# Kernel optimization log

Hardware: AMD Instinct MI355X
Metric: run time of the kernel (lower is better)

The kernel has to match this reference:

```python
import jax, jax.numpy as jnp
import numpy as np

N_ITER = 5  # from init_kwargs


def setup_inputs() -> dict:
    key = jax.random.key(0)
    k1, k2 = jax.random.split(key)
    K, F, B = 4, 513, 4000
    Xr = jax.random.normal(k1, (K, F, B), dtype=jnp.float32)
    Xi = jax.random.normal(k2, (K, F, B), dtype=jnp.float32)
    return {"Xr": Xr, "Xi": Xi}


def _auxiva(X):
    # X: complex64 (K, F, B)
    K, F, B = X.shape
    # XXh[i,j,f,b] = X[i,f,b] * conj(X[j,f,b])
    XXh = jnp.einsum('ifb,jfb->ijfb', X, X.conj())
    Wh = jnp.tile(jnp.eye(K, dtype=X.dtype)[None], (F, 1, 1))  # (F, K, K)
    for _ in range(N_ITER):
        Y = jnp.einsum('fsc,cfb->sfb', Wh, X)          # demix: (K, F, B)
        r = jnp.linalg.norm(Y, axis=1)                  # (K, B), real
        phi = 1.0 / (2.0 * r)                           # laplace contrast
        # V[k,i,j,f] = mean_b phi[k,b] * XXh[i,j,f,b]  (avoid (K,K,K,F,B) blowup)
        V = jnp.einsum('kb,ijfb->kijf', phi.astype(X.dtype), XXh) / B
        for k in range(K):                              # sequential IP updates
            M = jnp.einsum('fik,kjf->fij', Wh, V[k])    # (F, K, K)
            w = jnp.linalg.inv(M)[:, :, k].conj()       # (F, K)
            denom = jnp.sqrt(jnp.einsum('fc,ckf,fk->f', w, V[k], w.conj()))
            Wh = Wh.at[:, k, :].set(w / denom[:, None])
    Y = jnp.einsum('fsc,cfb->sfb', Wh, X)
    scale = jnp.linalg.inv(Wh)[:, :, 0]                 # projection back: (F, K)
    return jnp.einsum('sfb,fs->sfb', Y, scale)


def reference(Xr, Xi):
    X = (Xr + 1j * Xi).astype(jnp.complex64)
    return _auxiva(X)
```

## Files before the change

kernel.cpp:

```cpp
#include <hip/hip_runtime.h>
#include <hip/hip_bf16.h>
#include <math.h>

#define K 4
#define F 513
#define B 4000
#define NIT 5
#define FB (F*B)
#define KB (K*B)
#define FCH 8
#define NFC 65

__device__ float2 g_Wh[F*16];
__device__ float2 g_V[64*F];
__device__ float2 g_scale[F*4];
__device__ float  g_r2p[NFC*KB];
__device__ float  g_r2[KB];

struct cd { double re, im; };
__device__ inline cd mkcd(double r, double i){ cd z; z.re=r; z.im=i; return z; }
__device__ inline cd cmul(cd a, cd b){ return mkcd(a.re*b.re - a.im*b.im, a.re*b.im + a.im*b.re); }
__device__ inline cd cadd(cd a, cd b){ return mkcd(a.re+b.re, a.im+b.im); }
__device__ inline cd csub(cd a, cd b){ return mkcd(a.re-b.re, a.im-b.im); }
__device__ inline cd conj_(cd a){ return mkcd(a.re, -a.im); }
__device__ inline cd cdiv(cd a, cd b){
  double d = b.re*b.re + b.im*b.im;
  return mkcd((a.re*b.re + a.im*b.im)/d, (a.im*b.re - a.re*b.im)/d);
}

__device__ inline void invcol4(const cd M[4][4], int kk, cd x[4]){
  int r0 = (kk==0)?1:0;
  int r1 = (kk<=1)?2:1;
  int r2 = (kk<=2)?3:2;
  cd cof[4];
  #pragma unroll
  for (int i=0;i<4;++i){
    int c0 = (i==0)?1:0;
    int c1 = (i<=1)?2:1;
    int c2 = (i<=2)?3:2;
    cd m = cadd(csub(cmul(M[r0][c0], csub(cmul(M[r1][c1],M[r2][c2]), cmul(M[r1][c2],M[r2][c1]))),
                     cmul(M[r0][c1], csub(cmul(M[r1][c0],M[r2][c2]), cmul(M[r1][c2],M[r2][c0])))),
                cmul(M[r0][c2], csub(cmul(M[r1][c0],M[r2][c1]), cmul(M[r1][c1],M[r2][c0]))));
    if ((kk+i)&1) m = mkcd(-m.re,-m.im);
    cof[i] = m;
  }
  cd det = mkcd(0.0,0.0);
  #pragma unroll
  for (int i=0;i<4;++i) det = cadd(det, cmul(M[kk][i], cof[i]));
  cd idet = cdiv(mkcd(1.0,0.0), det);
  #pragma unroll
  for (int i=0;i<4;++i) x[i] = cmul(cof[i], idet);
}


__global__ void init_kernel(){
  int t = blockIdx.x*blockDim.x + threadIdx.x;
  if (t < F*16){
    int sc = t & 15; int s = sc >> 2, c = sc & 3;
    g_Wh[t] = make_float2(s==c ? 1.0f : 0.0f, 0.0f);
  }
}

__global__ __launch_bounds__(256) void demix_part_kernel(
    const float* __restrict__ Xr, const float* __restrict__ Xi){
  int b = blockIdx.x*blockDim.x + threadIdx.x;
  if (b >= B) return;
  int y = blockIdx.y;
  int f0 = y*FCH, f1 = min(f0+FCH, F);
  float acc[K];
  #pragma unroll
  for (int s=0;s<K;++s) acc[s]=0.0f;
  for (int f=f0; f<f1; ++f){
    float xr[K], xi[K];
    #pragma unroll
    for (int c=0;c<K;++c){ int idx=c*FB + f*B + b; xr[c]=Xr[idx]; xi[c]=Xi[idx]; }
    const float2* w = g_Wh + f*16;
    #pragma unroll
    for (int s=0;s<K;++s){
      float yr=0.0f, yi=0.0f;
      #pragma unroll
      for (int c=0;c<K;++c){
        float2 ww = w[s*4+c];
        yr += ww.x*xr[c] - ww.y*xi[c];
        yi += ww.x*xi[c] + ww.y*xr[c];
      }
      acc[s] += yr*yr + yi*yi;
    }
  }
  #pragma unroll
  for (int s=0;s<K;++s) g_r2p[y*KB + s*B + b] = acc[s];
}

__global__ __launch_bounds__(256) void reduce_r2_kernel(){
  int t = blockIdx.x*blockDim.x + threadIdx.x;
  if (t >= KB) return;
  float s = 0.0f;
  #pragma unroll 5
  for (int y=0; y<NFC; ++y) s += g_r2p[y*KB + t];
  g_r2[t] = s;
}

__global__ __launch_bounds__(256) void v_kernel(
    const float* __restrict__ Xr, const float* __restrict__ Xi){
  int f = blockIdx.x;
  int tid = threadIdx.x;
  float acc[64];
  #pragma unroll
  for (int q=0;q<64;++q) acc[q]=0.0f;

  for (int b=tid; b<B; b+=256){
    float phi[K];
    #pragma unroll
    for (int k=0;k<K;++k) phi[k] = 0.5f / sqrtf(g_r2[k*B+b]);
    float xr[K], xi[K];
    #pragma unroll
    for (int c=0;c<K;++c){ int idx=c*FB + f*B + b; xr[c]=Xr[idx]; xi[c]=Xi[idx]; }
    float p[16];
    #pragma unroll
    for (int i=0;i<4;++i) p[i] = xr[i]*xr[i] + xi[i]*xi[i];
    int s = 4;
    #pragma unroll
    for (int i=0;i<4;++i){
      #pragma unroll
      for (int j=i+1;j<4;++j){
        p[s++] = xr[i]*xr[j] + xi[i]*xi[j];
        p[s++] = xi[i]*xr[j] - xr[i]*xi[j];
      }
    }
    #pragma unroll
    for (int k=0;k<K;++k){
      #pragma unroll
      for (int q=0;q<16;++q) acc[k*16+q] += phi[k]*p[q];
    }
  }

  __shared__ float part[4*64];
  __shared__ float red[64];
  int lane = tid & 63, wave = tid >> 6;
  #pragma unroll
  for (int q=0;q<64;++q){
    float v = acc[q];
    for (int off=32; off>0; off>>=1) v += __shfl_down(v, off);
    if (lane == 0) part[wave*64+q] = v;
  }
  __syncthreads();
  if (tid < 64){
    red[tid] = (part[tid] + part[64+tid] + part[128+tid] + part[192+tid]) * (1.0f/B);
  }
  __syncthreads();
  if (tid < 64){
    int k = tid >> 4, ij = tid & 15, i = ij >> 2, j = ij & 3;
    float re, im;
    if (i == j){ re = red[k*16 + i]; im = 0.0f; }
    else {
      int a = min(i,j), c2 = max(i,j);
      int pidx = (a==0) ? (c2-1) : ((a==1) ? (c2+1) : 5);
      re = red[k*16 + 4 + 2*pidx];
      im = red[k*16 + 5 + 2*pidx];
      if (i > j) im = -im;
    }
    g_V[(unsigned)tid*F + f] = make_float2(re, im);
  }
}

__global__ __launch_bounds__(64) void update_kernel(int do_scale){
  int f = blockIdx.x*blockDim.x + threadIdx.x;
  if (f >= F) return;
  cd W[4][4];
  #pragma unroll
  for (int s=0;s<4;++s)
    #pragma unroll
    for (int c=0;c<4;++c){ float2 w = g_Wh[f*16+s*4+c]; W[s][c] = mkcd((double)w.x,(double)w.y); }

  #pragma unroll
  for (int k=0;k<4;++k){
    cd Vk[4][4];
    #pragma unroll
    for (int i=0;i<4;++i)
      #pragma unroll
      for (int j=0;j<4;++j){ float2 v = g_V[((k*4+i)*4+j)*F + f]; Vk[i][j] = mkcd((double)v.x,(double)v.y); }
    cd M[4][4];
    #pragma unroll
    for (int i=0;i<4;++i)
      #pragma unroll
      for (int j=0;j<4;++j){
        cd s = mkcd(0.0,0.0);
        #pragma unroll
        for (int c=0;c<4;++c) s = cadd(s, cmul(W[i][c], Vk[c][j]));
        M[i][j] = s;
      }
    cd x[4];
    invcol4(M, k, x);
    cd w[4];
    #pragma unroll
    for (int c=0;c<4;++c) w[c] = conj_(x[c]);
    double dre = 0.0;
    #pragma unroll
    for (int j=0;j<4;++j){
      cd tj = mkcd(0.0,0.0);
      #pragma unroll
      for (int c=0;c<4;++c) tj = cadd(tj, cmul(w[c], Vk[c][j]));
      dre += tj.re*w[j].re + tj.im*w[j].im;
    }
    double inv_denom = rsqrt(dre > 0.0 ? dre : 1e-300);
    #pragma unroll
    for (int c=0;c<4;++c) W[k][c] = mkcd(w[c].re*inv_denom, w[c].im*inv_denom);
  }
  #pragma unroll
  for (int s=0;s<4;++s)
    #pragma unroll
    for (int c=0;c<4;++c) g_Wh[f*16+s*4+c] = make_float2((float)W[s][c].re, (float)W[s][c].im);

  if (do_scale){
    cd x[4];
    invcol4(W, 0, x);
    #pragma unroll
    for (int s=0;s<4;++s) g_scale[f*4+s] = make_float2((float)x[s].re, (float)x[s].im);
  }
}

__global__ __launch_bounds__(256) void final_kernel(
    const float* __restrict__ Xr, const float* __restrict__ Xi,
    __hip_bfloat162* __restrict__ out){
  int b = blockIdx.x*blockDim.x + threadIdx.x;
  if (b >= B) return;
  int f0 = blockIdx.y*FCH, f1 = min(f0+FCH, F);
  for (int f=f0; f<f1; ++f){
    float xr[K], xi[K];
    #pragma unroll
    for (int c=0;c<K;++c){ int idx=c*FB + f*B + b; xr[c]=Xr[idx]; xi[c]=Xi[idx]; }
    const float2* w = g_Wh + f*16;
    #pragma unroll
    for (int s=0;s<K;++s){
      float yr=0.0f, yi=0.0f;
      #pragma unroll
      for (int c=0;c<K;++c){
        float2 ww = w[s*4+c];
        yr += ww.x*xr[c] - ww.y*xi[c];
        yi += ww.x*xi[c] + ww.y*xr[c];
      }
      float2 sc = g_scale[f*4+s];
      __hip_bfloat162 o;
      o.x = __float2bfloat16(yr*sc.x - yi*sc.y);
      o.y = __float2bfloat16(yr*sc.y + yi*sc.x);
      out[s*FB + f*B + b] = o;
    }
  }
}

extern "C" void kernel_launch(void* const* d_in, const int* in_sizes, int n_in,
                              void* d_out, int out_size, void* d_ws, size_t ws_size,
                              hipStream_t stream){
  const float* Xr = (const float*)d_in[1];
  const float* Xi = (const float*)d_in[0];
  __hip_bfloat162* out = (__hip_bfloat162*)d_out;

  init_kernel<<<33, 256, 0, stream>>>();
  dim3 gD((B + 255)/256, NFC);
  for (int it=0; it<NIT; ++it){
    demix_part_kernel<<<gD, 256, 0, stream>>>(Xr, Xi);
    reduce_r2_kernel<<<(KB + 255)/256, 256, 0, stream>>>();
    v_kernel<<<F, 256, 0, stream>>>(Xr, Xi);
    update_kernel<<<(F + 63)/64, 64, 0, stream>>>(it == NIT-1 ? 1 : 0);
  }
  final_kernel<<<gD, 256, 0, stream>>>(Xr, Xi, out);
}
```

Measured before the change: 432.1 us.

## Split V accumulation over batch chunks and use butterfly shuffle reduction

The V kernel grid is split across four batch chunks, so it launches 2052 blocks instead of 513, and the partial covariances are summed in the update kernel. The 64 separate shuffle-down reductions are replaced by a recursive-halving xor butterfly, which leaves one value per lane and needs far fewer shuffles. phi is now computed once in the reduction kernel instead of per f-block. The risks are extra global partial buffers and extra loads in the update kernel, and the launch bound of 4 may cause register spills for the 64 accumulators.

```diff
diff --git a/kernel.cpp b/kernel.cpp
--- a/kernel.cpp
+++ b/kernel.cpp
@@ -10,12 +10,14 @@
 #define KB (K*B)
 #define FCH 8
 #define NFC 65
+#define NBC 4
+#define BCH (B/NBC)
 
 __device__ float2 g_Wh[F*16];
-__device__ float2 g_V[64*F];
+__device__ float2 g_Vp[NBC*64*F];
 __device__ float2 g_scale[F*4];
 __device__ float  g_r2p[NFC*KB];
-__device__ float  g_r2[KB];
+__device__ float  g_phi[KB];
 
 struct cd { double re, im; };
 __device__ inline cd mkcd(double r, double i){ cd z; z.re=r; z.im=i; return z; }
@@ -91,27 +93,29 @@
   for (int s=0;s<K;++s) g_r2p[y*KB + s*B + b] = acc[s];
 }
 
-__global__ __launch_bounds__(256) void reduce_r2_kernel(){
+__global__ __launch_bounds__(256) void phi_kernel(){
   int t = blockIdx.x*blockDim.x + threadIdx.x;
   if (t >= KB) return;
   float s = 0.0f;
   #pragma unroll 5
   for (int y=0; y<NFC; ++y) s += g_r2p[y*KB + t];
-  g_r2[t] = s;
-}
-
-__global__ __launch_bounds__(256) void v_kernel(
+  g_phi[t] = 0.5f / sqrtf(s);
+}
+
+__global__ __launch_bounds__(256, 4) void v_kernel(
     const float* __restrict__ Xr, const float* __restrict__ Xi){
   int f = blockIdx.x;
+  int y = blockIdx.y;
   int tid = threadIdx.x;
   float acc[64];
   #pragma unroll
   for (int q=0;q<64;++q) acc[q]=0.0f;
 
-  for (int b=tid; b<B; b+=256){
+  int b0 = y*BCH;
+  for (int b = b0 + tid; b < b0 + BCH; b += 256){
     float phi[K];
     #pragma unroll
-    for (int k=0;k<K;++k) phi[k] = 0.5f / sqrtf(g_r2[k*B+b]);
+    for (int k=0;k<K;++k) phi[k] = g_phi[k*B+b];
     float xr[K], xi[K];
     #pragma unroll
     for (int c=0;c<K;++c){ int idx=c*FB + f*B + b; xr[c]=Xr[idx]; xi[c]=Xi[idx]; }
@@ -134,15 +138,22 @@
     }
   }
 
+  int lane = tid & 63, wave = tid >> 6;
+  #pragma unroll
+  for (int d=0; d<6; ++d){
+    const int sh = 1<<d;
+    const bool hi = (lane & sh) != 0;
+    #pragma unroll
+    for (int m=0; m<(32>>d); ++m){
+      float keep = hi ? acc[2*m+1] : acc[2*m];
+      float send = hi ? acc[2*m]   : acc[2*m+1];
+      acc[m] = keep + __shfl_xor(send, sh);
+    }
+  }
+
   __shared__ float part[4*64];
   __shared__ float red[64];
-  int lane = tid & 63, wave = tid >> 6;
-  #pragma unroll
-  for (int q=0;q<64;++q){
-    float v = acc[q];
-    for (int off=32; off>0; off>>=1) v += __shfl_down(v, off);
-    if (lane == 0) part[wave*64+q] = v;
-  }
+  part[wave*64 + lane] = acc[0];
   __syncthreads();
   if (tid < 64){
     red[tid] = (part[tid] + part[64+tid] + part[128+tid] + part[192+tid]) * (1.0f/B);
@@ -159,7 +170,7 @@
       im = red[k*16 + 5 + 2*pidx];
       if (i > j) im = -im;
     }
-    g_V[(unsigned)tid*F + f] = make_float2(re, im);
+    g_Vp[(y*64 + (unsigned)tid)*F + f] = make_float2(re, im);
   }
 }
 
@@ -178,7 +189,15 @@
     #pragma unroll
     for (int i=0;i<4;++i)
       #pragma unroll
-      for (int j=0;j<4;++j){ float2 v = g_V[((k*4+i)*4+j)*F + f]; Vk[i][j] = mkcd((double)v.x,(double)v.y); }
+      for (int j=0;j<4;++j){
+        float2 vv = make_float2(0.0f, 0.0f);
+        #pragma unroll
+        for (int y=0;y<NBC;++y){
+          float2 t2 = g_Vp[(y*64 + (k*4+i)*4 + j)*F + f];
+          vv.x += t2.x; vv.y += t2.y;
+        }
+        Vk[i][j] = mkcd((double)vv.x,(double)vv.y);
+      }
     cd M[4][4];
     #pragma unroll
     for (int i=0;i<4;++i)
@@ -257,10 +276,11 @@
 
   init_kernel<<<33, 256, 0, stream>>>();
   dim3 gD((B + 255)/256, NFC);
+  dim3 gV(F, NBC);
   for (int it=0; it<NIT; ++it){
     demix_part_kernel<<<gD, 256, 0, stream>>>(Xr, Xi);
-    reduce_r2_kernel<<<(KB + 255)/256, 256, 0, stream>>>();
-    v_kernel<<<F, 256, 0, stream>>>(Xr, Xi);
+    phi_kernel<<<(KB + 255)/256, 256, 0, stream>>>();
+    v_kernel<<<gV, 256, 0, stream>>>(Xr, Xi);
     update_kernel<<<(F + 63)/64, 64, 0, stream>>>(it == NIT-1 ? 1 : 0);
   }
   final_kernel<<<gD, 256, 0, stream>>>(Xr, Xi, out);
```

After: 356.1 us. -17.6%, faster.
